# Performance work log

Hardware: AMD Instinct MI355X
Metric: run time of the kernel (lower is better)

## Reference

```python
import jax, jax.numpy as jnp
import numpy as np
from jax import lax

B, T, D, H = 64, 512, 512, 1024


def setup_inputs() -> dict:
    key = jax.random.key(0)
    k1, k2, k3 = jax.random.split(key, 3)
    X = jax.random.normal(k1, (B, T, D), dtype=jnp.float32)
    # TF GRUCell params: gate kernel/bias (reset+update), candidate kernel/bias.
    gate_kernel = jax.random.normal(k2, (D + H, 2 * H), dtype=jnp.float32) * 0.02
    gate_bias = jnp.ones((2 * H,), dtype=jnp.float32)  # TF default bias init = 1.0
    cand_kernel = jax.random.normal(k3, (D + H, H), dtype=jnp.float32) * 0.02
    cand_bias = jnp.zeros((H,), dtype=jnp.float32)
    return {"X": X, "gate_kernel": gate_kernel, "gate_bias": gate_bias,
            "cand_kernel": cand_kernel, "cand_bias": cand_bias}


def reference(X, gate_kernel, gate_bias, cand_kernel, cand_bias):
    # Faithful TF GRUCell unrolled over time (static_rnn semantics, zero init state).
    b, t, d = X.shape
    h0 = jnp.zeros((b, cand_bias.shape[0]), dtype=X.dtype)

    def step(h, x):
        # gates: sigmoid([x, h] @ Wg + bg) -> split into reset r, update u
        gi = jnp.concatenate([x, h], axis=1) @ gate_kernel + gate_bias
        r, u = jnp.split(jax.nn.sigmoid(gi), 2, axis=1)
        # candidate: tanh([x, r*h] @ Wc + bc)
        c = jnp.tanh(jnp.concatenate([x, r * h], axis=1) @ cand_kernel + cand_bias)
        new_h = u * h + (1.0 - u) * c
        return new_h, new_h

    xs = jnp.swapaxes(X, 0, 1)  # [T, B, D]
    _, ys = lax.scan(step, h0, xs)
    return jnp.swapaxes(ys, 0, 1)  # [B, T, H]
```

## Files before the change

kernel.cpp:

```cpp
#include <hip/hip_runtime.h>


typedef __attribute__((ext_vector_type(8))) short          s16x8;
typedef __attribute__((ext_vector_type(4))) float          f32x4;
typedef __attribute__((ext_vector_type(4))) unsigned short us4;
typedef __attribute__((ext_vector_type(8))) unsigned short us8;
typedef unsigned long long ull;
typedef unsigned short us;

#define TT 512
#define DD 512
#define HH 1024
#define WPGE 1032
#define ASTR 1032
#define XSTR 520
#define O_ASH (64 * WPGE)
#define O_XS  (O_ASH + 8 * ASTR)
#define O_USH (O_XS + 8 * XSTR)
#define O_PS  (O_USH + 576)
#define LDS_BYTES ((O_PS + 640) * 2)
#define XP_LDSB (64 * 520 * 2 + 16 * 520 * 2)

#define W_FL   0
#define W_HB   32768
#define W_RHB  163840
#define W_END  294912
#define POLLCAP (1 << 17)

__device__ __forceinline__ us f2b(float f) {
  unsigned u = __float_as_uint(f);
  u += 0x7FFFu + ((u >> 16) & 1u);
  return (us)(u >> 16);
}
__device__ __forceinline__ float b2f(us b) { return __uint_as_float(((unsigned)b) << 16); }

__device__ __forceinline__ void waitf(const unsigned* f, unsigned e, int lane, bool& bad) {
  if (bad) return;
  const unsigned* p = f + (lane & 31) * 16;
  int n = 0;
  for (;;) {
    unsigned v = (lane < 32)
        ? __hip_atomic_load(p, __ATOMIC_RELAXED, __HIP_MEMORY_SCOPE_AGENT) : e;
    if (__all((int)(v >= e))) return;
    if (++n > POLLCAP) { bad = true; return; }
    __builtin_amdgcn_s_sleep(1);
  }
}

__device__ __forceinline__ void stage(const us* g, us* A, int row8, int lp) {
  const ull* p = (const ull*)(g + (size_t)row8 * HH) + lp;
  ull r[8];
  #pragma unroll
  for (int j = 0; j < 8; ++j)
    r[j] = __hip_atomic_load(p + j * 32, __ATOMIC_RELAXED, __HIP_MEMORY_SCOPE_AGENT);
  us* d = A + row8 * ASTR + lp * 4;
  #pragma unroll
  for (int j = 0; j < 8; ++j) *(ull*)(d + j * 128) = r[j];
}

__device__ __forceinline__ ull quad_pack(float v0, float v1, float v2, float v3, int q) {
  unsigned p01 = (unsigned)f2b(v0) | ((unsigned)f2b(v1) << 16);
  unsigned p23 = (unsigned)f2b(v2) | ((unsigned)f2b(v3) << 16);
  unsigned o01 = __shfl_xor(p01, 2);
  unsigned o23 = __shfl_xor(p23, 2);
  unsigned x = (q < 2) ? p01 : o23;
  unsigned y = (q < 2) ? o01 : p23;
  unsigned ux = __shfl_xor(x, 1);
  unsigned uy = __shfl_xor(y, 1);
  unsigned w0, w1;
  if (q & 1) { w0 = (ux >> 16) | (x & 0xFFFF0000u); w1 = (uy >> 16) | (y & 0xFFFF0000u); }
  else       { w0 = (x & 0xFFFFu) | (ux << 16);     w1 = (y & 0xFFFFu) | (uy << 16); }
  return (ull)w0 | ((ull)w1 << 32);
}

extern "C" __global__ void __launch_bounds__(256, 1)
gru_persistent(const float* __restrict__ X, const float* __restrict__ GK,
               const float* __restrict__ GB, const float* __restrict__ CK,
               const float* __restrict__ CB, float* __restrict__ Y,
               unsigned char* __restrict__ ws) {
  extern __shared__ us lds[];
  us*    Wg  = lds;
  us*    Ash = lds + O_ASH;
  us*    Xs  = lds + O_XS;
  float* ush = (float*)(lds + O_USH);
  float* ps  = (float*)(lds + O_PS);

  const int tid = threadIdx.x, bid = blockIdx.x;
  const int isl = bid & 7, iw = bid >> 3;
  const int lane = tid & 63, w = tid >> 6;
  const int r16 = lane & 15, g4 = lane >> 4;
  const int row8 = tid >> 5, lp = tid & 31;
  const int cb = iw * 32;
  const int half = w & 1;
  const int tlB = w >> 1, khB = w & 1;

  unsigned* hfl = (unsigned*)(ws + (size_t)isl * 4096);
  unsigned* rfl = hfl + 512;
  us* hbI  = (us*)(ws + W_HB)  + (size_t)(isl * 8) * HH;
  us* rhbI = (us*)(ws + W_RHB) + (size_t)(isl * 8) * HH;

  {
    const int c = tid & 63;
    const size_t gcol = (c < 32) ? (size_t)(cb + c) : (size_t)(1024 + cb + (c - 32));
    for (int k = tid >> 6; k < 1024; k += 4)
      Wg[c * WPGE + k] = f2b(GK[(size_t)(512 + k) * 2048 + gcol]);
  }
  s16x8 wx[16], wc[16];
  {
    const size_t gx = (size_t)(cb + half * 16 + r16) + (w >= 2 ? 1024 : 0);
    #pragma unroll
    for (int c2 = 0; c2 < 16; ++c2) {
      us t0[8];
      #pragma unroll
      for (int e = 0; e < 8; ++e)
        t0[e] = f2b(GK[(size_t)(c2 * 32 + g4 * 8 + e) * 2048 + gx]);
      wx[c2] = (s16x8){(short)t0[0],(short)t0[1],(short)t0[2],(short)t0[3],
                       (short)t0[4],(short)t0[5],(short)t0[6],(short)t0[7]};
    }
  }
  {
    const size_t ccol = (size_t)(cb + tlB * 16 + r16);
    #pragma unroll
    for (int c2 = 0; c2 < 16; ++c2) {
      us t0[8];
      #pragma unroll
      for (int e = 0; e < 8; ++e)
        t0[e] = f2b(CK[(size_t)(512 + khB * 512 + c2 * 32 + g4 * 8 + e) * 1024 + ccol]);
      wc[c2] = (s16x8){(short)t0[0],(short)t0[1],(short)t0[2],(short)t0[3],
                       (short)t0[4],(short)t0[5],(short)t0[6],(short)t0[7]};
    }
  }
  const float biasG = (w < 2) ? GB[cb + half * 16 + r16]
                              : GB[1024 + cb + half * 16 + r16];
  const float biasC = CB[cb + tlB * 16 + r16];

  float hreg[4] = {0.f, 0.f, 0.f, 0.f};
  bool bad = false;
  float4 px0, px1, px2, px3;
  {
    const float* s = X + (size_t)(isl * 8 + row8) * TT * DD + lp * 16;
    px0 = *(const float4*)s;       px1 = *(const float4*)(s + 4);
    px2 = *(const float4*)(s + 8); px3 = *(const float4*)(s + 12);
  }

  for (int t = 0; t < TT; ++t) {
    {
      us* xd = Xs + row8 * XSTR + lp * 16;
      us8 v0 = { f2b(px0.x), f2b(px0.y), f2b(px0.z), f2b(px0.w),
                 f2b(px1.x), f2b(px1.y), f2b(px1.z), f2b(px1.w) };
      us8 v1 = { f2b(px2.x), f2b(px2.y), f2b(px2.z), f2b(px2.w),
                 f2b(px3.x), f2b(px3.y), f2b(px3.z), f2b(px3.w) };
      *(us8*)xd = v0; *(us8*)(xd + 8) = v1;
    }
    __syncthreads();

    f32x4 a0 = {0.f,0.f,0.f,0.f}, a1 = {0.f,0.f,0.f,0.f};
    {
      const us* arX = Xs + (r16 & 7) * XSTR;
      #pragma unroll
      for (int c2 = 0; c2 < 16; c2 += 2) {
        a0 = __builtin_amdgcn_mfma_f32_16x16x32_bf16(
               *(const s16x8*)(arX + c2 * 32 + g4 * 8), wx[c2], a0, 0, 0, 0);
        a1 = __builtin_amdgcn_mfma_f32_16x16x32_bf16(
               *(const s16x8*)(arX + (c2 + 1) * 32 + g4 * 8), wx[c2 + 1], a1, 0, 0, 0);
      }
    }
    waitf(hfl, (unsigned)t, lane, bad);
    stage(hbI, Ash, row8, lp);
    __syncthreads();

    {
      const us* arB = Ash + (r16 & 7) * ASTR;
      const us* brB = Wg + (w * 16 + r16) * WPGE + g4 * 8;
      #pragma unroll
      for (int c2 = 0; c2 < 32; c2 += 2) {
        a0 = __builtin_amdgcn_mfma_f32_16x16x32_bf16(
               *(const s16x8*)(arB + c2 * 32 + g4 * 8),
               *(const s16x8*)(brB + c2 * 32), a0, 0, 0, 0);
        a1 = __builtin_amdgcn_mfma_f32_16x16x32_bf16(
               *(const s16x8*)(arB + (c2 + 1) * 32 + g4 * 8),
               *(const s16x8*)(brB + (c2 + 1) * 32), a1, 0, 0, 0);
      }
    }
    if (g4 < 2) {
      if (w < 2) {
        const int colR = cb + half * 16 + r16;
        float rh[4];
        #pragma unroll
        for (int i = 0; i < 4; ++i) {
          float gg = 1.f / (1.f + __expf(-(a0[i] + a1[i] + biasG)));
          rh[i] = gg * b2f(Ash[(g4 * 4 + i) * ASTR + colR]);
        }
        ull tv = quad_pack(rh[0], rh[1], rh[2], rh[3], r16 & 3);
        __hip_atomic_store(
            (ull*)(rhbI + (size_t)(g4 * 4 + (r16 & 3)) * HH + cb + half * 16 + (r16 & ~3)),
            tv, __ATOMIC_RELAXED, __HIP_MEMORY_SCOPE_AGENT);
      } else {
        const int uc = half * 16 + r16;
        #pragma unroll
        for (int i = 0; i < 4; ++i)
          ush[(g4 * 4 + i) * 36 + uc] = 1.f / (1.f + __expf(-(a0[i] + a1[i] + biasG)));
      }
    }
    __syncthreads();
    if (tid == 0)
      __hip_atomic_store(rfl + iw * 16, (unsigned)(t + 1),
                         __ATOMIC_RELAXED, __HIP_MEMORY_SCOPE_AGENT);

    float xc[4];
    if (khB == 0 && g4 < 2) {
      const int colC = cb + tlB * 16 + r16;
      #pragma unroll
      for (int i = 0; i < 4; ++i)
        xc[i] = Y[((size_t)(isl * 8 + g4 * 4 + i) * TT + t) * HH + colC];
    }
    waitf(rfl, (unsigned)(t + 1), lane, bad);
    stage(rhbI, Ash, row8, lp);
    __syncthreads();

    f32x4 c0 = {0.f,0.f,0.f,0.f}, c1 = {0.f,0.f,0.f,0.f};
    {
      const us* arC = Ash + (r16 & 7) * ASTR + khB * 512;
      #pragma unroll
      for (int c2 = 0; c2 < 16; c2 += 2) {
        c0 = __builtin_amdgcn_mfma_f32_16x16x32_bf16(
               *(const s16x8*)(arC + c2 * 32 + g4 * 8), wc[c2], c0, 0, 0, 0);
        c1 = __builtin_amdgcn_mfma_f32_16x16x32_bf16(
               *(const s16x8*)(arC + (c2 + 1) * 32 + g4 * 8), wc[c2 + 1], c1, 0, 0, 0);
      }
    }
    if (khB == 1 && g4 < 2) {
      #pragma unroll
      for (int i = 0; i < 4; ++i)
        ps[tlB * 160 + (g4 * 4 + i) * 20 + r16] = c0[i] + c1[i];
    }
    __syncthreads();
    if (khB == 0 && g4 < 2) {
      const int colC = cb + tlB * 16 + r16;
      float hn[4];
      #pragma unroll
      for (int i = 0; i < 4; ++i) {
        int rr = g4 * 4 + i;
        float cv = tanhf(c0[i] + c1[i] + ps[tlB * 160 + rr * 20 + r16] + xc[i] + biasC);
        float uu = ush[rr * 36 + tlB * 16 + r16];
        hn[i] = uu * hreg[i] + (1.f - uu) * cv;
        hreg[i] = hn[i];
        Y[((size_t)(isl * 8 + rr) * TT + t) * HH + colC] = hn[i];
      }
      ull tv = quad_pack(hn[0], hn[1], hn[2], hn[3], r16 & 3);
      __hip_atomic_store(
          (ull*)(hbI + (size_t)(g4 * 4 + (r16 & 3)) * HH + cb + tlB * 16 + (r16 & ~3)),
          tv, __ATOMIC_RELAXED, __HIP_MEMORY_SCOPE_AGENT);
    }
    if (t + 1 < TT) {
      const float* s = X + ((size_t)(isl * 8 + row8) * TT + (t + 1)) * DD + lp * 16;
      px0 = *(const float4*)s;       px1 = *(const float4*)(s + 4);
      px2 = *(const float4*)(s + 8); px3 = *(const float4*)(s + 12);
    }
    __syncthreads();
    if (tid == 0)
      __hip_atomic_store(hfl + iw * 16, (unsigned)(t + 1),
                         __ATOMIC_RELAXED, __HIP_MEMORY_SCOPE_AGENT);
  }
  if (bad && tid == 0) Y[1] = 31337.f;
}

extern "C" __global__ void __launch_bounds__(256, 1)
xproj_c(const float* __restrict__ X, const float* __restrict__ CK,
        float* __restrict__ Y) {
  extern __shared__ us lds[];
  us* Bc  = lds;
  us* Axs = lds + 64 * 520;
  const int tid = threadIdx.x, lane = tid & 63, w = tid >> 6;
  const int r16 = lane & 15, g4 = lane >> 4;
  const int nt = blockIdx.x & 15, mb = blockIdx.x >> 4;
  const int n0 = nt * 64;
  const int srow = tid >> 4, slp = tid & 15;

  {
    const int c4 = (tid & 15) * 4;
    for (int k = tid >> 4; k < 512; k += 16) {
      float4 v = *(const float4*)(CK + (size_t)k * HH + n0 + c4);
      Bc[(c4 + 0) * 520 + k] = f2b(v.x);  Bc[(c4 + 1) * 520 + k] = f2b(v.y);
      Bc[(c4 + 2) * 520 + k] = f2b(v.z);  Bc[(c4 + 3) * 520 + k] = f2b(v.w);
    }
  }
  __syncthreads();

  for (int mt = 0; mt < 32; ++mt) {
    const size_t m0 = (size_t)mb * 512 + mt * 16;
    {
      const float* src = X + (m0 + srow) * 512 + slp * 4;
      us* d = Axs + srow * 520 + slp * 4;
      #pragma unroll
      for (int j = 0; j < 8; ++j) {
        float4 v = *(const float4*)(src + j * 64);
        us4 p = { f2b(v.x), f2b(v.y), f2b(v.z), f2b(v.w) };
        *(us4*)(d + j * 64) = p;
      }
    }
    __syncthreads();
    const int ci = w;
    f32x4 ac0 = {0.f,0.f,0.f,0.f}, ac1 = {0.f,0.f,0.f,0.f};
    const us* ar = Axs + r16 * 520 + g4 * 8;
    const us* bc = Bc + (ci * 16 + r16) * 520 + g4 * 8;
    #pragma unroll
    for (int f = 0; f < 16; f += 2) {
      ac0 = __builtin_amdgcn_mfma_f32_16x16x32_bf16(
              *(const s16x8*)(ar + f * 32), *(const s16x8*)(bc + f * 32), ac0, 0,0,0);
      ac1 = __builtin_amdgcn_mfma_f32_16x16x32_bf16(
              *(const s16x8*)(ar + f * 32 + 32), *(const s16x8*)(bc + f * 32 + 32), ac1, 0,0,0);
    }
    #pragma unroll
    for (int i = 0; i < 4; ++i)
      Y[(m0 + g4 * 4 + i) * HH + n0 + ci * 16 + r16] = ac0[i] + ac1[i];
    __syncthreads();
  }
}

extern "C" __global__ void gru_sentinel(float* out, float v) {
  if (blockIdx.x == 0 && threadIdx.x == 0) out[0] = v;
}

extern "C" void kernel_launch(void* const* d_in, const int* in_sizes, int n_in,
                              void* d_out, int out_size, void* d_ws, size_t ws_size,
                              hipStream_t stream) {
  const float* X  = (const float*)d_in[0];
  const float* GK = (const float*)d_in[1];
  const float* GB = (const float*)d_in[2];
  const float* CK = (const float*)d_in[3];
  const float* CB = (const float*)d_in[4];
  float* Y = (float*)d_out;
  unsigned char* wsb = (unsigned char*)d_ws;

  if (ws_size < (size_t)W_END) {
    gru_sentinel<<<1, 64, 0, stream>>>(Y, 1000.f + (float)(ws_size >> 20));
    return;
  }

  hipMemsetAsync(d_ws, 0, W_END, stream);

  (void)hipFuncSetAttribute((const void*)xproj_c,
                            hipFuncAttributeMaxDynamicSharedMemorySize, XP_LDSB);
  xproj_c<<<dim3(16 * 64), dim3(256), XP_LDSB, stream>>>(X, CK, Y);

  (void)hipFuncSetAttribute((const void*)gru_persistent,
                            hipFuncAttributeMaxDynamicSharedMemorySize, LDS_BYTES);
  gru_persistent<<<dim3(256), dim3(256), LDS_BYTES, stream>>>(X, GK, GB, CK, CB, Y, wsb);
}
```

Before: 2.991 ms.

## Map workgroups to XCDs and use XCD-local L2 sync with per-wave flags

At startup each workgroup reads its XCD id and takes a slot through an atomic counter. If every XCD gets exactly 32 workgroups, the batch slice is assigned by XCD so that all cooperating workgroups share one L2. A probe handshake then checks that sc0 stores plus buffer_inv loads give coherent visibility inside the XCD, and if so the per-step h/rh exchanges and flags use these cheaper L2-local operations instead of agent-scope atomics. The block-wide barriers before each flag publish are replaced by per-wave drains with two split flags, which cuts synchronization latency on the serial recurrence. This adds startup overhead and relies on the hardware placement and memory-model assumptions, with fallback paths if the checks fail.

```diff
diff --git a/kernel.cpp b/kernel.cpp
--- a/kernel.cpp
+++ b/kernel.cpp
@@ -21,11 +21,16 @@
 #define LDS_BYTES ((O_PS + 640) * 2)
 #define XP_LDSB (64 * 520 * 2 + 16 * 520 * 2)
 
-#define W_FL   0
-#define W_HB   32768
-#define W_RHB  163840
-#define W_END  294912
-#define POLLCAP (1 << 17)
+#define W_CNT  0
+#define W_PRB  1024
+#define W_OKS  17408
+#define W_VER  18432
+#define W_FL   20480
+#define W_HB   86016
+#define W_RHB  217088
+#define W_END  348160
+#define CAP_AG (1 << 17)
+#define CAP_LC (1 << 16)
 
 __device__ __forceinline__ us f2b(float f) {
   unsigned u = __float_as_uint(f);
@@ -34,25 +39,54 @@
 }
 __device__ __forceinline__ float b2f(us b) { return __uint_as_float(((unsigned)b) << 16); }
 
-__device__ __forceinline__ void waitf(const unsigned* f, unsigned e, int lane, bool& bad) {
+__device__ __forceinline__ void inv_wait() {
+  asm volatile("buffer_inv\n\ts_waitcnt vmcnt(0)" ::: "memory");
+}
+__device__ __forceinline__ void drain_vm() {
+  asm volatile("s_waitcnt vmcnt(0)" ::: "memory");
+}
+__device__ __forceinline__ void st4_sc0(void* p, unsigned v) {
+  asm volatile("global_store_dword %0, %1, off sc0" :: "v"(p), "v"(v) : "memory");
+}
+__device__ __forceinline__ void st8_sc0(void* p, ull v) {
+  asm volatile("global_store_dwordx2 %0, %1, off sc0" :: "v"(p), "v"(v) : "memory");
+}
+
+__device__ __forceinline__ void pub8(ull* p, ull v, bool loc) {
+  if (loc) st8_sc0(p, v);
+  else __hip_atomic_store(p, v, __ATOMIC_RELAXED, __HIP_MEMORY_SCOPE_AGENT);
+}
+__device__ __forceinline__ void pubfl(unsigned* p, unsigned v, bool loc) {
+  if (loc) st4_sc0(p, v);
+  else __hip_atomic_store(p, v, __ATOMIC_RELAXED, __HIP_MEMORY_SCOPE_AGENT);
+}
+__device__ __forceinline__ void waitf2(const unsigned* fA, const unsigned* fB,
+                                       unsigned e, int lane, bool loc, bool& bad) {
   if (bad) return;
-  const unsigned* p = f + (lane & 31) * 16;
+  const unsigned* p = (lane < 32) ? (fA + lane * 16) : (fB + (lane - 32) * 16);
   int n = 0;
+  const int cap = loc ? CAP_LC : CAP_AG;
   for (;;) {
-    unsigned v = (lane < 32)
-        ? __hip_atomic_load(p, __ATOMIC_RELAXED, __HIP_MEMORY_SCOPE_AGENT) : e;
+    unsigned v;
+    if (loc) { inv_wait(); v = *(volatile const unsigned*)p; }
+    else v = __hip_atomic_load(p, __ATOMIC_RELAXED, __HIP_MEMORY_SCOPE_AGENT);
     if (__all((int)(v >= e))) return;
-    if (++n > POLLCAP) { bad = true; return; }
+    if (++n > cap) { bad = true; return; }
     __builtin_amdgcn_s_sleep(1);
   }
 }
-
-__device__ __forceinline__ void stage(const us* g, us* A, int row8, int lp) {
+__device__ __forceinline__ void stage(const us* g, us* A, int row8, int lp, bool loc) {
   const ull* p = (const ull*)(g + (size_t)row8 * HH) + lp;
   ull r[8];
-  #pragma unroll
-  for (int j = 0; j < 8; ++j)
-    r[j] = __hip_atomic_load(p + j * 32, __ATOMIC_RELAXED, __HIP_MEMORY_SCOPE_AGENT);
+  if (loc) {
+    inv_wait();
+    #pragma unroll
+    for (int j = 0; j < 8; ++j) r[j] = *(volatile const ull*)(p + j * 32);
+  } else {
+    #pragma unroll
+    for (int j = 0; j < 8; ++j)
+      r[j] = __hip_atomic_load(p + j * 32, __ATOMIC_RELAXED, __HIP_MEMORY_SCOPE_AGENT);
+  }
   us* d = A + row8 * ASTR + lp * 4;
   #pragma unroll
   for (int j = 0; j < 8; ++j) *(ull*)(d + j * 128) = r[j];
@@ -86,16 +120,122 @@
   float* ps  = (float*)(lds + O_PS);
 
   const int tid = threadIdx.x, bid = blockIdx.x;
-  const int isl = bid & 7, iw = bid >> 3;
   const int lane = tid & 63, w = tid >> 6;
   const int r16 = lane & 15, g4 = lane >> 4;
   const int row8 = tid >> 5, lp = tid & 31;
-  const int cb = iw * 32;
   const int half = w & 1;
   const int tlB = w >> 1, khB = w & 1;
 
-  unsigned* hfl = (unsigned*)(ws + (size_t)isl * 4096);
-  unsigned* rfl = hfl + 512;
+  unsigned* cnt = (unsigned*)(ws + W_CNT);
+  unsigned* prb = (unsigned*)(ws + W_PRB);
+  unsigned* oks = (unsigned*)(ws + W_OKS);
+  unsigned* ver = (unsigned*)(ws + W_VER);
+
+  if (tid == 0) {
+    unsigned xcd = (unsigned)__builtin_amdgcn_s_getreg((31 << 11) | 20) & 7u;
+    unsigned slot = __hip_atomic_fetch_add(cnt + xcd, 1u, __ATOMIC_RELAXED,
+                                           __HIP_MEMORY_SCOPE_AGENT);
+    int n = 0; bool okr = true;
+    for (;;) {
+      unsigned s = 0;
+      #pragma unroll
+      for (int x = 0; x < 8; ++x)
+        s += __hip_atomic_load(cnt + x, __ATOMIC_RELAXED, __HIP_MEMORY_SCOPE_AGENT);
+      if (s >= 256u) break;
+      if (++n > (1 << 20)) { okr = false; break; }
+      __builtin_amdgcn_s_sleep(2);
+    }
+    bool dyn = okr;
+    if (okr) {
+      #pragma unroll
+      for (int x = 0; x < 8; ++x)
+        dyn = dyn && (__hip_atomic_load(cnt + x, __ATOMIC_RELAXED,
+                                        __HIP_MEMORY_SCOPE_AGENT) == 32u);
+    }
+    unsigned uisl, uiw, um;
+    if (dyn) { uisl = xcd; uiw = slot; um = 1u; }
+    else     { uisl = (unsigned)(bid & 7); uiw = (unsigned)(bid >> 3); um = 0u; }
+    ush[0] = __uint_as_float(uisl);
+    ush[1] = __uint_as_float(uiw);
+    ush[2] = __uint_as_float(um);
+  }
+  __syncthreads();
+  const int  isl = (int)__float_as_uint(ush[0]);
+  const int  iw  = (int)__float_as_uint(ush[1]);
+  const bool dynmode = __float_as_uint(ush[2]) != 0u;
+  __syncthreads();
+  const int cb = iw * 32;
+
+  bool loc = false;
+  if (dynmode) {
+    unsigned* myslot = prb + (size_t)(isl * 32 + iw) * 16;
+    if (w == 0) {
+      bool okl = true;
+      for (unsigned r = 1; r <= 16u && okl; ++r) {
+        if (lane == 0) {
+          st8_sc0(myslot + 2, ((ull)r << 32) | r);
+          st4_sc0(myslot, r);
+        }
+        int n = 0;
+        for (;;) {
+          inv_wait();
+          bool ok = true;
+          if (lane < 32) {
+            const unsigned* q = prb + (size_t)(isl * 32 + lane) * 16;
+            unsigned f = *(volatile const unsigned*)q;
+            ull      d = *(volatile const ull*)(q + 2);
+            ok = (f >= r) && ((unsigned)(d & 0xFFFFFFFFull) >= r);
+          }
+          if (__all((int)ok)) break;
+          if (++n > (1 << 14)) { okl = false; break; }
+          __builtin_amdgcn_s_sleep(2);
+        }
+      }
+      if (lane == 0) ush[4] = __uint_as_float(okl ? 1u : 0u);
+    }
+    __syncthreads();
+    const bool okwg = __float_as_uint(ush[4]) != 0u;
+    __syncthreads();
+    if (tid == 0)
+      __hip_atomic_store(oks + isl * 32 + iw, okwg ? 1u : 2u,
+                         __ATOMIC_RELAXED, __HIP_MEMORY_SCOPE_AGENT);
+    if (iw == 0 && w == 0) {
+      bool allok = true;
+      if (lane < 32) {
+        unsigned v = 0; int n = 0;
+        for (;;) {
+          v = __hip_atomic_load(oks + isl * 32 + lane, __ATOMIC_RELAXED,
+                                __HIP_MEMORY_SCOPE_AGENT);
+          if (v) break;
+          if (++n > (1 << 20)) { v = 2u; break; }
+          __builtin_amdgcn_s_sleep(4);
+        }
+        allok = (v == 1u);
+      }
+      bool uni = __all((int)allok);
+      if (lane == 0)
+        __hip_atomic_store(ver + isl, uni ? 1u : 2u, __ATOMIC_RELAXED,
+                           __HIP_MEMORY_SCOPE_AGENT);
+    }
+    if (tid == 0) {
+      unsigned m = 0; int n = 0;
+      for (;;) {
+        m = __hip_atomic_load(ver + isl, __ATOMIC_RELAXED, __HIP_MEMORY_SCOPE_AGENT);
+        if (m) break;
+        if (++n > (1 << 20)) { m = 2u; break; }
+        __builtin_amdgcn_s_sleep(4);
+      }
+      ush[5] = __uint_as_float(m);
+    }
+    __syncthreads();
+    loc = (__float_as_uint(ush[5]) == 1u);
+    __syncthreads();
+  }
+
+  unsigned* rA = (unsigned*)(ws + W_FL + (size_t)isl * 8192);
+  unsigned* rB = rA + 512;
+  unsigned* hA = rA + 1024;
+  unsigned* hB = rA + 1536;
   us* hbI  = (us*)(ws + W_HB)  + (size_t)(isl * 8) * HH;
   us* rhbI = (us*)(ws + W_RHB) + (size_t)(isl * 8) * HH;
 
@@ -165,8 +305,8 @@
                *(const s16x8*)(arX + (c2 + 1) * 32 + g4 * 8), wx[c2 + 1], a1, 0, 0, 0);
       }
     }
-    waitf(hfl, (unsigned)t, lane, bad);
-    stage(hbI, Ash, row8, lp);
+    waitf2(hA, hB, (unsigned)t, lane, loc, bad);
+    stage(hbI, Ash, row8, lp, loc);
     __syncthreads();
 
     {
@@ -192,9 +332,8 @@
           rh[i] = gg * b2f(Ash[(g4 * 4 + i) * ASTR + colR]);
         }
         ull tv = quad_pack(rh[0], rh[1], rh[2], rh[3], r16 & 3);
-        __hip_atomic_store(
-            (ull*)(rhbI + (size_t)(g4 * 4 + (r16 & 3)) * HH + cb + half * 16 + (r16 & ~3)),
-            tv, __ATOMIC_RELAXED, __HIP_MEMORY_SCOPE_AGENT);
+        pub8((ull*)(rhbI + (size_t)(g4 * 4 + (r16 & 3)) * HH + cb + half * 16 + (r16 & ~3)),
+             tv, loc);
       } else {
         const int uc = half * 16 + r16;
         #pragma unroll
@@ -202,10 +341,8 @@
           ush[(g4 * 4 + i) * 36 + uc] = 1.f / (1.f + __expf(-(a0[i] + a1[i] + biasG)));
       }
     }
-    __syncthreads();
-    if (tid == 0)
-      __hip_atomic_store(rfl + iw * 16, (unsigned)(t + 1),
-                         __ATOMIC_RELAXED, __HIP_MEMORY_SCOPE_AGENT);
+    if (w == 0) { drain_vm(); if (lane == 0) pubfl(rA + iw * 16, (unsigned)(t + 1), loc); }
+    if (w == 1) { drain_vm(); if (lane == 0) pubfl(rB + iw * 16, (unsigned)(t + 1), loc); }
 
     float xc[4];
     if (khB == 0 && g4 < 2) {
@@ -214,8 +351,8 @@
       for (int i = 0; i < 4; ++i)
         xc[i] = Y[((size_t)(isl * 8 + g4 * 4 + i) * TT + t) * HH + colC];
     }
-    waitf(rfl, (unsigned)(t + 1), lane, bad);
-    stage(rhbI, Ash, row8, lp);
+    waitf2(rA, rB, (unsigned)(t + 1), lane, loc, bad);
+    stage(rhbI, Ash, row8, lp, loc);
     __syncthreads();
 
     f32x4 c0 = {0.f,0.f,0.f,0.f}, c1 = {0.f,0.f,0.f,0.f};
@@ -248,19 +385,17 @@
         Y[((size_t)(isl * 8 + rr) * TT + t) * HH + colC] = hn[i];
       }
       ull tv = quad_pack(hn[0], hn[1], hn[2], hn[3], r16 & 3);
-      __hip_atomic_store(
-          (ull*)(hbI + (size_t)(g4 * 4 + (r16 & 3)) * HH + cb + tlB * 16 + (r16 & ~3)),
-          tv, __ATOMIC_RELAXED, __HIP_MEMORY_SCOPE_AGENT);
-    }
+      pub8((ull*)(hbI + (size_t)(g4 * 4 + (r16 & 3)) * HH + cb + tlB * 16 + (r16 & ~3)),
+           tv, loc);
+    }
+    if (w == 0) { drain_vm(); if (lane == 0) pubfl(hA + iw * 16, (unsigned)(t + 1), loc); }
+    if (w == 2) { drain_vm(); if (lane == 0) pubfl(hB + iw * 16, (unsigned)(t + 1), loc); }
+
     if (t + 1 < TT) {
       const float* s = X + ((size_t)(isl * 8 + row8) * TT + (t + 1)) * DD + lp * 16;
       px0 = *(const float4*)s;       px1 = *(const float4*)(s + 4);
       px2 = *(const float4*)(s + 8); px3 = *(const float4*)(s + 12);
     }
-    __syncthreads();
-    if (tid == 0)
-      __hip_atomic_store(hfl + iw * 16, (unsigned)(t + 1),
-                         __ATOMIC_RELAXED, __HIP_MEMORY_SCOPE_AGENT);
   }
   if (bad && tid == 0) Y[1] = 31337.f;
 }
```

Measured after the change: 3.260 ms. 9.0% more time.

## Publish per-wave readiness flags instead of block barrier before flag store

Applied to the files above, without the earlier changes.

Replaces the block-wide __syncthreads followed by a single thread's flag store with per-wave flags. Each producing wave drains its own outstanding stores with s_waitcnt vmcnt(0) and then publishes its own flag. Consumers poll both flag arrays in one wave, using 32 lanes for each. This takes two block barriers off the critical path of every recurrent step, at the cost of twice as many flags to poll. It also relies on vmcnt draining being enough to make the relaxed stores visible to other blocks.

```diff
diff --git a/kernel.cpp b/kernel.cpp
--- a/kernel.cpp
+++ b/kernel.cpp
@@ -22,10 +22,10 @@
 #define XP_LDSB (64 * 520 * 2 + 16 * 520 * 2)
 
 #define W_FL   0
-#define W_HB   32768
-#define W_RHB  163840
-#define W_END  294912
-#define POLLCAP (1 << 17)
+#define W_HB   65536
+#define W_RHB  196608
+#define W_END  327680
+#define CAP_AG (1 << 17)
 
 __device__ __forceinline__ us f2b(float f) {
   unsigned u = __float_as_uint(f);
@@ -34,19 +34,27 @@
 }
 __device__ __forceinline__ float b2f(us b) { return __uint_as_float(((unsigned)b) << 16); }
 
-__device__ __forceinline__ void waitf(const unsigned* f, unsigned e, int lane, bool& bad) {
+__device__ __forceinline__ void drain_vm() {
+  asm volatile("s_waitcnt vmcnt(0)" ::: "memory");
+}
+__device__ __forceinline__ void pubfl(unsigned* p, unsigned v) {
+  __hip_atomic_store(p, v, __ATOMIC_RELAXED, __HIP_MEMORY_SCOPE_AGENT);
+}
+__device__ __forceinline__ void pub8(ull* p, ull v) {
+  __hip_atomic_store(p, v, __ATOMIC_RELAXED, __HIP_MEMORY_SCOPE_AGENT);
+}
+__device__ __forceinline__ void waitf2(const unsigned* fA, const unsigned* fB,
+                                       unsigned e, int lane, bool& bad) {
   if (bad) return;
-  const unsigned* p = f + (lane & 31) * 16;
+  const unsigned* p = (lane < 32) ? (fA + lane * 16) : (fB + (lane - 32) * 16);
   int n = 0;
   for (;;) {
-    unsigned v = (lane < 32)
-        ? __hip_atomic_load(p, __ATOMIC_RELAXED, __HIP_MEMORY_SCOPE_AGENT) : e;
+    unsigned v = __hip_atomic_load(p, __ATOMIC_RELAXED, __HIP_MEMORY_SCOPE_AGENT);
     if (__all((int)(v >= e))) return;
-    if (++n > POLLCAP) { bad = true; return; }
+    if (++n > CAP_AG) { bad = true; return; }
     __builtin_amdgcn_s_sleep(1);
   }
 }
-
 __device__ __forceinline__ void stage(const us* g, us* A, int row8, int lp) {
   const ull* p = (const ull*)(g + (size_t)row8 * HH) + lp;
   ull r[8];
@@ -94,8 +102,10 @@
   const int half = w & 1;
   const int tlB = w >> 1, khB = w & 1;
 
-  unsigned* hfl = (unsigned*)(ws + (size_t)isl * 4096);
-  unsigned* rfl = hfl + 512;
+  unsigned* rA = (unsigned*)(ws + W_FL + (size_t)isl * 8192);
+  unsigned* rB = rA + 512;
+  unsigned* hA = rA + 1024;
+  unsigned* hB = rA + 1536;
   us* hbI  = (us*)(ws + W_HB)  + (size_t)(isl * 8) * HH;
   us* rhbI = (us*)(ws + W_RHB) + (size_t)(isl * 8) * HH;
 
@@ -165,7 +175,7 @@
                *(const s16x8*)(arX + (c2 + 1) * 32 + g4 * 8), wx[c2 + 1], a1, 0, 0, 0);
       }
     }
-    waitf(hfl, (unsigned)t, lane, bad);
+    waitf2(hA, hB, (unsigned)t, lane, bad);
     stage(hbI, Ash, row8, lp);
     __syncthreads();
 
@@ -192,9 +202,8 @@
           rh[i] = gg * b2f(Ash[(g4 * 4 + i) * ASTR + colR]);
         }
         ull tv = quad_pack(rh[0], rh[1], rh[2], rh[3], r16 & 3);
-        __hip_atomic_store(
-            (ull*)(rhbI + (size_t)(g4 * 4 + (r16 & 3)) * HH + cb + half * 16 + (r16 & ~3)),
-            tv, __ATOMIC_RELAXED, __HIP_MEMORY_SCOPE_AGENT);
+        pub8((ull*)(rhbI + (size_t)(g4 * 4 + (r16 & 3)) * HH + cb + half * 16 + (r16 & ~3)),
+             tv);
       } else {
         const int uc = half * 16 + r16;
         #pragma unroll
@@ -202,10 +211,8 @@
           ush[(g4 * 4 + i) * 36 + uc] = 1.f / (1.f + __expf(-(a0[i] + a1[i] + biasG)));
       }
     }
-    __syncthreads();
-    if (tid == 0)
-      __hip_atomic_store(rfl + iw * 16, (unsigned)(t + 1),
-                         __ATOMIC_RELAXED, __HIP_MEMORY_SCOPE_AGENT);
+    if (w == 0) { drain_vm(); if (lane == 0) pubfl(rA + iw * 16, (unsigned)(t + 1)); }
+    if (w == 1) { drain_vm(); if (lane == 0) pubfl(rB + iw * 16, (unsigned)(t + 1)); }
 
     float xc[4];
     if (khB == 0 && g4 < 2) {
@@ -214,7 +221,7 @@
       for (int i = 0; i < 4; ++i)
         xc[i] = Y[((size_t)(isl * 8 + g4 * 4 + i) * TT + t) * HH + colC];
     }
-    waitf(rfl, (unsigned)(t + 1), lane, bad);
+    waitf2(rA, rB, (unsigned)(t + 1), lane, bad);
     stage(rhbI, Ash, row8, lp);
     __syncthreads();
 
@@ -248,19 +255,17 @@
         Y[((size_t)(isl * 8 + rr) * TT + t) * HH + colC] = hn[i];
       }
       ull tv = quad_pack(hn[0], hn[1], hn[2], hn[3], r16 & 3);
-      __hip_atomic_store(
-          (ull*)(hbI + (size_t)(g4 * 4 + (r16 & 3)) * HH + cb + tlB * 16 + (r16 & ~3)),
-          tv, __ATOMIC_RELAXED, __HIP_MEMORY_SCOPE_AGENT);
-    }
+      pub8((ull*)(hbI + (size_t)(g4 * 4 + (r16 & 3)) * HH + cb + tlB * 16 + (r16 & ~3)),
+           tv);
+    }
+    if (w == 0) { drain_vm(); if (lane == 0) pubfl(hA + iw * 16, (unsigned)(t + 1)); }
+    if (w == 2) { drain_vm(); if (lane == 0) pubfl(hB + iw * 16, (unsigned)(t + 1)); }
+
     if (t + 1 < TT) {
       const float* s = X + ((size_t)(isl * 8 + row8) * TT + (t + 1)) * DD + lp * 16;
       px0 = *(const float4*)s;       px1 = *(const float4*)(s + 4);
       px2 = *(const float4*)(s + 8); px3 = *(const float4*)(s + 12);
     }
-    __syncthreads();
-    if (tid == 0)
-      __hip_atomic_store(hfl + iw * 16, (unsigned)(t + 1),
-                         __ATOMIC_RELAXED, __HIP_MEMORY_SCOPE_AGENT);
   }
   if (bad && tid == 0) Y[1] = 31337.f;
 }
```

Measured after the change: 3.609 ms. +20.7%, slower.
